# Performance work log

Measured on AMD Instinct MI355X. Metric: run time of the kernel, lower is better.

Reference implementation:

```python
import jax, jax.numpy as jnp
import numpy as np

N, D, H, E, A = 524288, 64, 128, 8, 18
BN_EPS = 1e-5


def setup_inputs() -> dict:
    key = jax.random.key(0)
    ks = jax.random.split(key, 4)
    X = jax.random.normal(ks[0], (N, D), dtype=jnp.float32)
    W1 = jax.random.normal(ks[1], (H, D), dtype=jnp.float32) * 0.05
    b1 = jnp.zeros((H,), dtype=jnp.float32)
    gamma = jnp.ones((H,), dtype=jnp.float32)
    beta = jnp.zeros((H,), dtype=jnp.float32)
    rmean = jnp.zeros((H,), dtype=jnp.float32)
    rvar = jnp.ones((H,), dtype=jnp.float32)
    W2 = jax.random.normal(ks[2], (E, H), dtype=jnp.float32) * 0.05
    b2 = jnp.zeros((E,), dtype=jnp.float32)
    We = jax.random.normal(ks[3], (E, A, D), dtype=jnp.float32) * 0.05
    return {"X": X, "W1": W1, "b1": b1, "gamma": gamma, "beta": beta,
            "rmean": rmean, "rvar": rvar, "W2": W2, "b2": b2, "We": We}


def reference(X, W1, b1, gamma, beta, rmean, rvar, W2, b2, We):
    # Gating MLP: Linear -> BatchNorm1d (eval, running stats) -> ReLU -> Linear
    h = X @ W1.T + b1                                   # [N, H]
    h = gamma * (h - rmean) * jax.lax.rsqrt(rvar + BN_EPS) + beta
    h = jax.nn.relu(h)
    logits = h @ W2.T + b2                              # [N, E]
    # Straight-through hard routing
    y_soft = jax.nn.softmax(logits, axis=-1)
    y_hard = jax.nn.one_hot(jnp.argmax(y_soft, axis=-1), E, dtype=y_soft.dtype)
    ret = y_hard - jax.lax.stop_gradient(y_soft) + y_soft  # [N, E]
    # All experts at once: [N,E,A], then mask-weighted sum over experts
    expert_out = jnp.einsum('nd,ead->nea', X, We)
    output = jnp.einsum('nea,ne->na', expert_out, ret)     # [N, A]
    return output, ret
```

## Files before the change

### kernel.cpp

```cpp
#include <hip/hip_runtime.h>
#include <hip/hip_bf16.h>
#include <math.h>

#define DD 64
#define HH 128
#define EE 8
#define AA 18
#define BN_EPS 1e-5f

#define TIE_MARGIN 5e-5f

#define WE_STRIDE 1156

__global__ __launch_bounds__(256, 2) void moe_hot(
    const float* __restrict__ X,
    const float* __restrict__ W1,
    const float* __restrict__ b1,
    const float* __restrict__ gamma,
    const float* __restrict__ beta,
    const float* __restrict__ rmean,
    const float* __restrict__ rvar,
    const float* __restrict__ W2,
    const float* __restrict__ b2,
    const float* __restrict__ We,
    float* __restrict__ out,
    float* __restrict__ ret,
    int* __restrict__ flags,
    int Ntot)
{
    __shared__ float sWe[EE * WE_STRIDE];

    const int tid = threadIdx.x;
    const int n = blockIdx.x * 256 + tid;

    float4 x[16];
    if (n < Ntot) {
        const float4* xv = (const float4*)(X + (size_t)n * DD);
        #pragma unroll
        for (int k = 0; k < 16; ++k) x[k] = xv[k];
    }

    for (int i = tid; i < EE * AA * DD; i += 256) {
        int e = i / (AA * DD);
        int r = i - e * (AA * DD);
        sWe[e * WE_STRIDE + r] = We[i];
    }

    __syncthreads();

    if (n >= Ntot) return;

    float logits[EE];
    #pragma unroll
    for (int e = 0; e < EE; ++e) logits[e] = b2[e];

    #pragma unroll 2
    for (int j = 0; j < HH; ++j) {
        const float4* wv = (const float4*)(W1 + j * DD);
        float s0 = 0.f, s1 = 0.f, s2 = 0.f, s3 = 0.f;
        #pragma unroll
        for (int k = 0; k < 16; ++k) {
            float4 w = wv[k];
            s0 = fmaf(x[k].x, w.x, s0);
            s1 = fmaf(x[k].y, w.y, s1);
            s2 = fmaf(x[k].z, w.z, s2);
            s3 = fmaf(x[k].w, w.w, s3);
        }
        float h = ((s0 + s1) + (s2 + s3)) + b1[j];
        float sc = gamma[j] * rsqrtf(rvar[j] + BN_EPS);
        float hb = fmaf(h - rmean[j], sc, beta[j]);
        hb = fmaxf(hb, 0.f);
        #pragma unroll
        for (int e = 0; e < EE; ++e)
            logits[e] = fmaf(hb, W2[e * HH + j], logits[e]);
    }

    int emax = 0;
    float lmax = logits[0];
    #pragma unroll
    for (int e = 1; e < EE; ++e) {
        if (logits[e] > lmax) { lmax = logits[e]; emax = e; }
    }
    float second = -INFINITY;
    #pragma unroll
    for (int e = 0; e < EE; ++e) {
        if (e != emax && logits[e] > second) second = logits[e];
    }
    flags[n] = (lmax - second < TIE_MARGIN) ? 1 : 0;

    float4* retv = (float4*)(ret + (size_t)n * EE);
    retv[0] = make_float4(emax == 0 ? 1.f : 0.f, emax == 1 ? 1.f : 0.f,
                          emax == 2 ? 1.f : 0.f, emax == 3 ? 1.f : 0.f);
    retv[1] = make_float4(emax == 4 ? 1.f : 0.f, emax == 5 ? 1.f : 0.f,
                          emax == 6 ? 1.f : 0.f, emax == 7 ? 1.f : 0.f);

    const float* wexp = &sWe[emax * WE_STRIDE];
    float outv[AA];
    #pragma unroll
    for (int a = 0; a < AA; ++a) {
        const float4* wv = (const float4*)(wexp + a * DD);
        float s0 = 0.f, s1 = 0.f, s2 = 0.f, s3 = 0.f;
        #pragma unroll
        for (int k = 0; k < 16; ++k) {
            float4 w = wv[k];
            s0 = fmaf(x[k].x, w.x, s0);
            s1 = fmaf(x[k].y, w.y, s1);
            s2 = fmaf(x[k].z, w.z, s2);
            s3 = fmaf(x[k].w, w.w, s3);
        }
        outv[a] = (s0 + s1) + (s2 + s3);
    }
    float2* ov = (float2*)(out + (size_t)n * AA);
    #pragma unroll
    for (int a2 = 0; a2 < 9; ++a2)
        ov[a2] = make_float2(outv[2 * a2], outv[2 * a2 + 1]);
}

__global__ __launch_bounds__(256, 2) void moe_fix(
    const float* __restrict__ X,
    const float* __restrict__ W1,
    const float* __restrict__ b1,
    const float* __restrict__ gamma,
    const float* __restrict__ beta,
    const float* __restrict__ rmean,
    const float* __restrict__ rvar,
    const float* __restrict__ W2,
    const float* __restrict__ b2,
    const float* __restrict__ We,
    float* __restrict__ out,
    float* __restrict__ ret,
    const int* __restrict__ flags,
    int Ntot)
{
    const int n = blockIdx.x * 256 + threadIdx.x;
    if (n >= Ntot) return;
    if (flags[n] == 0) return;

    const float* xg = X + (size_t)n * DD;

    double ld[EE];
    #pragma unroll
    for (int e = 0; e < EE; ++e) ld[e] = (double)b2[e];
    for (int j = 0; j < HH; ++j) {
        const float* w = W1 + j * DD;
        double hd = 0.0;
        for (int k = 0; k < DD; ++k)
            hd += (double)xg[k] * (double)w[k];
        hd += (double)b1[j];
        double sc = (double)gamma[j] / sqrt((double)rvar[j] + 1e-5);
        double hb = (hd - (double)rmean[j]) * sc + (double)beta[j];
        hb = hb > 0.0 ? hb : 0.0;
        #pragma unroll
        for (int e = 0; e < EE; ++e)
            ld[e] += hb * (double)W2[e * HH + j];
    }
    int emax = 0;
    double lm = ld[0];
    #pragma unroll
    for (int e = 1; e < EE; ++e) {
        if (ld[e] > lm) { lm = ld[e]; emax = e; }
    }

    float4* retv = (float4*)(ret + (size_t)n * EE);
    retv[0] = make_float4(emax == 0 ? 1.f : 0.f, emax == 1 ? 1.f : 0.f,
                          emax == 2 ? 1.f : 0.f, emax == 3 ? 1.f : 0.f);
    retv[1] = make_float4(emax == 4 ? 1.f : 0.f, emax == 5 ? 1.f : 0.f,
                          emax == 6 ? 1.f : 0.f, emax == 7 ? 1.f : 0.f);

    float4 x[16];
    const float4* xv = (const float4*)xg;
    #pragma unroll
    for (int k = 0; k < 16; ++k) x[k] = xv[k];

    const float* wexp = We + (size_t)emax * AA * DD;
    float outv[AA];
    #pragma unroll
    for (int a = 0; a < AA; ++a) {
        const float4* wv = (const float4*)(wexp + a * DD);
        float s0 = 0.f, s1 = 0.f, s2 = 0.f, s3 = 0.f;
        #pragma unroll
        for (int k = 0; k < 16; ++k) {
            float4 w = wv[k];
            s0 = fmaf(x[k].x, w.x, s0);
            s1 = fmaf(x[k].y, w.y, s1);
            s2 = fmaf(x[k].z, w.z, s2);
            s3 = fmaf(x[k].w, w.w, s3);
        }
        outv[a] = (s0 + s1) + (s2 + s3);
    }
    float2* ov = (float2*)(out + (size_t)n * AA);
    #pragma unroll
    for (int a2 = 0; a2 < 9; ++a2)
        ov[a2] = make_float2(outv[2 * a2], outv[2 * a2 + 1]);
}

extern "C" void kernel_launch(void* const* d_in, const int* in_sizes, int n_in,
                              void* d_out, int out_size, void* d_ws, size_t ws_size,
                              hipStream_t stream) {
    const float* X     = (const float*)d_in[0];
    const float* W1    = (const float*)d_in[1];
    const float* b1    = (const float*)d_in[2];
    const float* gamma = (const float*)d_in[3];
    const float* beta  = (const float*)d_in[4];
    const float* rmean = (const float*)d_in[5];
    const float* rvar  = (const float*)d_in[6];
    const float* W2    = (const float*)d_in[7];
    const float* b2    = (const float*)d_in[8];
    const float* We    = (const float*)d_in[9];

    const int Ntot = in_sizes[0] / DD;
    float* out = (float*)d_out;
    float* ret = out + (size_t)Ntot * AA;
    int* flags = (int*)d_ws;

    const int nblocks = (Ntot + 255) / 256;
    moe_hot<<<nblocks, 256, 0, stream>>>(
        X, W1, b1, gamma, beta, rmean, rvar, W2, b2, We, out, ret, flags, Ntot);
    moe_fix<<<nblocks, 256, 0, stream>>>(
        X, W1, b1, gamma, beta, rmean, rvar, W2, b2, We, out, ret, flags, Ntot);
}
```

Baseline: 795.7 us.

## Process two rows per thread and compact tie rows into an atomic worklist

Measured after the change: 670.5 us. 15.7% less time.

```diff
diff --git a/kernel.cpp b/kernel.cpp
--- a/kernel.cpp
+++ b/kernel.cpp
@@ -11,6 +11,10 @@
 #define TIE_MARGIN 5e-5f
 
 #define WE_STRIDE 1156
+
+#define ROWS_PER_BLOCK 512
+
+__global__ void zero_count(int* count) { if (threadIdx.x == 0) *count = 0; }
 
 __global__ __launch_bounds__(256, 2) void moe_hot(
     const float* __restrict__ X,
@@ -25,19 +29,26 @@
     const float* __restrict__ We,
     float* __restrict__ out,
     float* __restrict__ ret,
-    int* __restrict__ flags,
+    int* __restrict__ count,
+    int* __restrict__ list,
     int Ntot)
 {
     __shared__ float sWe[EE * WE_STRIDE];
 
     const int tid = threadIdx.x;
-    const int n = blockIdx.x * 256 + tid;
-
-    float4 x[16];
-    if (n < Ntot) {
-        const float4* xv = (const float4*)(X + (size_t)n * DD);
-        #pragma unroll
-        for (int k = 0; k < 16; ++k) x[k] = xv[k];
+    const int na = blockIdx.x * ROWS_PER_BLOCK + tid;
+    const int nb = na + 256;
+
+    float4 xa[16], xb[16];
+    if (na < Ntot) {
+        const float4* va = (const float4*)(X + (size_t)na * DD);
+        #pragma unroll
+        for (int k = 0; k < 16; ++k) xa[k] = va[k];
+    }
+    if (nb < Ntot) {
+        const float4* vb = (const float4*)(X + (size_t)nb * DD);
+        #pragma unroll
+        for (int k = 0; k < 16; ++k) xb[k] = vb[k];
     }
 
     for (int i = tid; i < EE * AA * DD; i += 256) {
@@ -48,75 +59,115 @@
 
     __syncthreads();
 
-    if (n >= Ntot) return;
-
-    float logits[EE];
-    #pragma unroll
-    for (int e = 0; e < EE; ++e) logits[e] = b2[e];
-
-    #pragma unroll 2
+    if (na >= Ntot) return;
+    const bool hasB = (nb < Ntot);
+
+    float lA[EE], lB[EE];
+    #pragma unroll
+    for (int e = 0; e < EE; ++e) { lA[e] = b2[e]; lB[e] = b2[e]; }
+
     for (int j = 0; j < HH; ++j) {
         const float4* wv = (const float4*)(W1 + j * DD);
-        float s0 = 0.f, s1 = 0.f, s2 = 0.f, s3 = 0.f;
+        float a0 = 0.f, a1 = 0.f, a2 = 0.f, a3 = 0.f;
+        float c0 = 0.f, c1 = 0.f, c2 = 0.f, c3 = 0.f;
         #pragma unroll
         for (int k = 0; k < 16; ++k) {
             float4 w = wv[k];
-            s0 = fmaf(x[k].x, w.x, s0);
-            s1 = fmaf(x[k].y, w.y, s1);
-            s2 = fmaf(x[k].z, w.z, s2);
-            s3 = fmaf(x[k].w, w.w, s3);
-        }
-        float h = ((s0 + s1) + (s2 + s3)) + b1[j];
+            a0 = fmaf(xa[k].x, w.x, a0);
+            a1 = fmaf(xa[k].y, w.y, a1);
+            a2 = fmaf(xa[k].z, w.z, a2);
+            a3 = fmaf(xa[k].w, w.w, a3);
+            c0 = fmaf(xb[k].x, w.x, c0);
+            c1 = fmaf(xb[k].y, w.y, c1);
+            c2 = fmaf(xb[k].z, w.z, c2);
+            c3 = fmaf(xb[k].w, w.w, c3);
+        }
         float sc = gamma[j] * rsqrtf(rvar[j] + BN_EPS);
-        float hb = fmaf(h - rmean[j], sc, beta[j]);
-        hb = fmaxf(hb, 0.f);
-        #pragma unroll
-        for (int e = 0; e < EE; ++e)
-            logits[e] = fmaf(hb, W2[e * HH + j], logits[e]);
-    }
-
-    int emax = 0;
-    float lmax = logits[0];
-    #pragma unroll
-    for (int e = 1; e < EE; ++e) {
-        if (logits[e] > lmax) { lmax = logits[e]; emax = e; }
-    }
-    float second = -INFINITY;
-    #pragma unroll
-    for (int e = 0; e < EE; ++e) {
-        if (e != emax && logits[e] > second) second = logits[e];
-    }
-    flags[n] = (lmax - second < TIE_MARGIN) ? 1 : 0;
-
-    float4* retv = (float4*)(ret + (size_t)n * EE);
-    retv[0] = make_float4(emax == 0 ? 1.f : 0.f, emax == 1 ? 1.f : 0.f,
-                          emax == 2 ? 1.f : 0.f, emax == 3 ? 1.f : 0.f);
-    retv[1] = make_float4(emax == 4 ? 1.f : 0.f, emax == 5 ? 1.f : 0.f,
-                          emax == 6 ? 1.f : 0.f, emax == 7 ? 1.f : 0.f);
-
-    const float* wexp = &sWe[emax * WE_STRIDE];
-    float outv[AA];
-    #pragma unroll
-    for (int a = 0; a < AA; ++a) {
-        const float4* wv = (const float4*)(wexp + a * DD);
-        float s0 = 0.f, s1 = 0.f, s2 = 0.f, s3 = 0.f;
-        #pragma unroll
-        for (int k = 0; k < 16; ++k) {
-            float4 w = wv[k];
-            s0 = fmaf(x[k].x, w.x, s0);
-            s1 = fmaf(x[k].y, w.y, s1);
-            s2 = fmaf(x[k].z, w.z, s2);
-            s3 = fmaf(x[k].w, w.w, s3);
-        }
-        outv[a] = (s0 + s1) + (s2 + s3);
-    }
-    float2* ov = (float2*)(out + (size_t)n * AA);
-    #pragma unroll
-    for (int a2 = 0; a2 < 9; ++a2)
-        ov[a2] = make_float2(outv[2 * a2], outv[2 * a2 + 1]);
+        float off = beta[j] - (rmean[j] - b1[j]) * sc;
+        float hA = fmaxf(fmaf(((a0 + a1) + (a2 + a3)), sc, off), 0.f);
+        float hB = fmaxf(fmaf(((c0 + c1) + (c2 + c3)), sc, off), 0.f);
+        #pragma unroll
+        for (int e = 0; e < EE; ++e) {
+            float w2 = W2[e * HH + j];
+            lA[e] = fmaf(hA, w2, lA[e]);
+            lB[e] = fmaf(hB, w2, lB[e]);
+        }
+    }
+
+    int eA = 0; float mA = lA[0];
+    #pragma unroll
+    for (int e = 1; e < EE; ++e) if (lA[e] > mA) { mA = lA[e]; eA = e; }
+    float sA = -INFINITY;
+    #pragma unroll
+    for (int e = 0; e < EE; ++e) if (e != eA && lA[e] > sA) sA = lA[e];
+    if (mA - sA < TIE_MARGIN) { int p = atomicAdd(count, 1); list[p] = na; }
+
+    int eB = 0; float mB = lB[0];
+    #pragma unroll
+    for (int e = 1; e < EE; ++e) if (lB[e] > mB) { mB = lB[e]; eB = e; }
+    float sB = -INFINITY;
+    #pragma unroll
+    for (int e = 0; e < EE; ++e) if (e != eB && lB[e] > sB) sB = lB[e];
+    if (hasB && (mB - sB < TIE_MARGIN)) { int p = atomicAdd(count, 1); list[p] = nb; }
+
+    float4* rA = (float4*)(ret + (size_t)na * EE);
+    rA[0] = make_float4(eA == 0 ? 1.f : 0.f, eA == 1 ? 1.f : 0.f,
+                        eA == 2 ? 1.f : 0.f, eA == 3 ? 1.f : 0.f);
+    rA[1] = make_float4(eA == 4 ? 1.f : 0.f, eA == 5 ? 1.f : 0.f,
+                        eA == 6 ? 1.f : 0.f, eA == 7 ? 1.f : 0.f);
+    if (hasB) {
+        float4* rB = (float4*)(ret + (size_t)nb * EE);
+        rB[0] = make_float4(eB == 0 ? 1.f : 0.f, eB == 1 ? 1.f : 0.f,
+                            eB == 2 ? 1.f : 0.f, eB == 3 ? 1.f : 0.f);
+        rB[1] = make_float4(eB == 4 ? 1.f : 0.f, eB == 5 ? 1.f : 0.f,
+                            eB == 6 ? 1.f : 0.f, eB == 7 ? 1.f : 0.f);
+    }
+
+    {
+        const float* wexp = &sWe[eA * WE_STRIDE];
+        float ov[AA];
+        #pragma unroll
+        for (int a = 0; a < AA; ++a) {
+            const float4* wv = (const float4*)(wexp + a * DD);
+            float s0 = 0.f, s1 = 0.f, s2 = 0.f, s3 = 0.f;
+            #pragma unroll
+            for (int k = 0; k < 16; ++k) {
+                float4 w = wv[k];
+                s0 = fmaf(xa[k].x, w.x, s0);
+                s1 = fmaf(xa[k].y, w.y, s1);
+                s2 = fmaf(xa[k].z, w.z, s2);
+                s3 = fmaf(xa[k].w, w.w, s3);
+            }
+            ov[a] = (s0 + s1) + (s2 + s3);
+        }
+        float2* po = (float2*)(out + (size_t)na * AA);
+        #pragma unroll
+        for (int q = 0; q < 9; ++q) po[q] = make_float2(ov[2 * q], ov[2 * q + 1]);
+    }
+    if (hasB) {
+        const float* wexp = &sWe[eB * WE_STRIDE];
+        float ov[AA];
+        #pragma unroll
+        for (int a = 0; a < AA; ++a) {
+            const float4* wv = (const float4*)(wexp + a * DD);
+            float s0 = 0.f, s1 = 0.f, s2 = 0.f, s3 = 0.f;
+            #pragma unroll
+            for (int k = 0; k < 16; ++k) {
+                float4 w = wv[k];
+                s0 = fmaf(xb[k].x, w.x, s0);
+                s1 = fmaf(xb[k].y, w.y, s1);
+                s2 = fmaf(xb[k].z, w.z, s2);
+                s3 = fmaf(xb[k].w, w.w, s3);
+            }
+            ov[a] = (s0 + s1) + (s2 + s3);
+        }
+        float2* po = (float2*)(out + (size_t)nb * AA);
+        #pragma unroll
+        for (int q = 0; q < 9; ++q) po[q] = make_float2(ov[2 * q], ov[2 * q + 1]);
+    }
 }
 
-__global__ __launch_bounds__(256, 2) void moe_fix(
+__global__ __launch_bounds__(256, 1) void moe_fix(
     const float* __restrict__ X,
     const float* __restrict__ W1,
     const float* __restrict__ b1,
@@ -129,69 +180,59 @@
     const float* __restrict__ We,
     float* __restrict__ out,
     float* __restrict__ ret,
-    const int* __restrict__ flags,
-    int Ntot)
+    const int* __restrict__ count,
+    const int* __restrict__ list)
 {
-    const int n = blockIdx.x * 256 + threadIdx.x;
-    if (n >= Ntot) return;
-    if (flags[n] == 0) return;
-
-    const float* xg = X + (size_t)n * DD;
-
-    double ld[EE];
-    #pragma unroll
-    for (int e = 0; e < EE; ++e) ld[e] = (double)b2[e];
-    for (int j = 0; j < HH; ++j) {
-        const float* w = W1 + j * DD;
-        double hd = 0.0;
-        for (int k = 0; k < DD; ++k)
-            hd += (double)xg[k] * (double)w[k];
-        hd += (double)b1[j];
-        double sc = (double)gamma[j] / sqrt((double)rvar[j] + 1e-5);
-        double hb = (hd - (double)rmean[j]) * sc + (double)beta[j];
-        hb = hb > 0.0 ? hb : 0.0;
-        #pragma unroll
-        for (int e = 0; e < EE; ++e)
-            ld[e] += hb * (double)W2[e * HH + j];
-    }
-    int emax = 0;
-    double lm = ld[0];
-    #pragma unroll
-    for (int e = 1; e < EE; ++e) {
-        if (ld[e] > lm) { lm = ld[e]; emax = e; }
-    }
-
-    float4* retv = (float4*)(ret + (size_t)n * EE);
-    retv[0] = make_float4(emax == 0 ? 1.f : 0.f, emax == 1 ? 1.f : 0.f,
-                          emax == 2 ? 1.f : 0.f, emax == 3 ? 1.f : 0.f);
-    retv[1] = make_float4(emax == 4 ? 1.f : 0.f, emax == 5 ? 1.f : 0.f,
-                          emax == 6 ? 1.f : 0.f, emax == 7 ? 1.f : 0.f);
-
-    float4 x[16];
-    const float4* xv = (const float4*)xg;
-    #pragma unroll
-    for (int k = 0; k < 16; ++k) x[k] = xv[k];
-
-    const float* wexp = We + (size_t)emax * AA * DD;
-    float outv[AA];
-    #pragma unroll
-    for (int a = 0; a < AA; ++a) {
-        const float4* wv = (const float4*)(wexp + a * DD);
-        float s0 = 0.f, s1 = 0.f, s2 = 0.f, s3 = 0.f;
-        #pragma unroll
-        for (int k = 0; k < 16; ++k) {
-            float4 w = wv[k];
-            s0 = fmaf(x[k].x, w.x, s0);
-            s1 = fmaf(x[k].y, w.y, s1);
-            s2 = fmaf(x[k].z, w.z, s2);
-            s3 = fmaf(x[k].w, w.w, s3);
-        }
-        outv[a] = (s0 + s1) + (s2 + s3);
-    }
-    float2* ov = (float2*)(out + (size_t)n * AA);
-    #pragma unroll
-    for (int a2 = 0; a2 < 9; ++a2)
-        ov[a2] = make_float2(outv[2 * a2], outv[2 * a2 + 1]);
+    const int nwork = *count;
+    for (int i = blockIdx.x * 256 + threadIdx.x; i < nwork; i += gridDim.x * 256) {
+        const int n = list[i];
+        const float* xg = X + (size_t)n * DD;
+
+        double ld[EE];
+        #pragma unroll
+        for (int e = 0; e < EE; ++e) ld[e] = (double)b2[e];
+        for (int j = 0; j < HH; ++j) {
+            const float* w = W1 + j * DD;
+            double hd = 0.0;
+            for (int k = 0; k < DD; ++k)
+                hd += (double)xg[k] * (double)w[k];
+            hd += (double)b1[j];
+            double sc = (double)gamma[j] / sqrt((double)rvar[j] + 1e-5);
+            double hb = (hd - (double)rmean[j]) * sc + (double)beta[j];
+            hb = hb > 0.0 ? hb : 0.0;
+            #pragma unroll
+            for (int e = 0; e < EE; ++e)
+                ld[e] += hb * (double)W2[e * HH + j];
+        }
+        int emax = 0;
+        double lm = ld[0];
+        #pragma unroll
+        for (int e = 1; e < EE; ++e) if (ld[e] > lm) { lm = ld[e]; emax = e; }
+
+        float4* rp = (float4*)(ret + (size_t)n * EE);
+        rp[0] = make_float4(emax == 0 ? 1.f : 0.f, emax == 1 ? 1.f : 0.f,
+                            emax == 2 ? 1.f : 0.f, emax == 3 ? 1.f : 0.f);
+        rp[1] = make_float4(emax == 4 ? 1.f : 0.f, emax == 5 ? 1.f : 0.f,
+                            emax == 6 ? 1.f : 0.f, emax == 7 ? 1.f : 0.f);
+
+        const float* wexp = We + (size_t)emax * AA * DD;
+        float ov[AA];
+        #pragma unroll
+        for (int a = 0; a < AA; ++a) {
+            const float* wr = wexp + a * DD;
+            float s0 = 0.f, s1 = 0.f, s2 = 0.f, s3 = 0.f;
+            for (int k = 0; k < 16; ++k) {
+                s0 = fmaf(xg[4 * k + 0], wr[4 * k + 0], s0);
+                s1 = fmaf(xg[4 * k + 1], wr[4 * k + 1], s1);
+                s2 = fmaf(xg[4 * k + 2], wr[4 * k + 2], s2);
+                s3 = fmaf(xg[4 * k + 3], wr[4 * k + 3], s3);
+            }
+            ov[a] = (s0 + s1) + (s2 + s3);
+        }
+        float* po = out + (size_t)n * AA;
+        #pragma unroll
+        for (int a = 0; a < AA; ++a) po[a] = ov[a];
+    }
 }
 
 extern "C" void kernel_launch(void* const* d_in, const int* in_sizes, int n_in,
@@ -211,11 +252,14 @@
     const int Ntot = in_sizes[0] / DD;
     float* out = (float*)d_out;
     float* ret = out + (size_t)Ntot * AA;
-    int* flags = (int*)d_ws;
-
-    const int nblocks = (Ntot + 255) / 256;
+    int* count = (int*)d_ws;
+    int* list  = (int*)d_ws + 16;
+
+    zero_count<<<1, 64, 0, stream>>>(count);
+
+    const int nblocks = (Ntot + ROWS_PER_BLOCK - 1) / ROWS_PER_BLOCK;
     moe_hot<<<nblocks, 256, 0, stream>>>(
-        X, W1, b1, gamma, beta, rmean, rvar, W2, b2, We, out, ret, flags, Ntot);
-    moe_fix<<<nblocks, 256, 0, stream>>>(
-        X, W1, b1, gamma, beta, rmean, rvar, W2, b2, We, out, ret, flags, Ntot);
+        X, W1, b1, gamma, beta, rmean, rvar, W2, b2, We, out, ret, count, list, Ntot);
+    moe_fix<<<16, 256, 0, stream>>>(
+        X, W1, b1, gamma, beta, rmean, rvar, W2, b2, We, out, ret, count, list);
 }
```
